# Performance work log

Measured on AMD Instinct MI355X. Metric: run time of the kernel, lower is better.

## Reference

```python
import jax, jax.numpy as jnp
import numpy as np

D = 256                      # covariance dim, hardcoded by bottleneck Conv2d(_, 256, 1)
ITER_N = 5                   # SqrtmLayer(output, 5)
_r, _c = np.triu_indices(D)
FLAT_IDX = jnp.asarray(_r * D + _c)   # upper-tri (incl. diag) indices into flattened d*d


def setup_inputs() -> dict:
    key = jax.random.key(0)
    ks = jax.random.split(key, 5)
    B, C, H, W = 64, 2048, 16, 16
    num_classes = 4
    feats = D * (D + 1) // 2  # 32896
    return {
        "features": jax.random.normal(ks[0], (B, C, H, W), jnp.float32),
        "w_bn": jax.random.normal(ks[1], (D, C), jnp.float32) * 0.02,
        "b_bn": jnp.zeros((D,), jnp.float32),
        "w_type": jax.random.normal(ks[2], (num_classes, feats), jnp.float32) * 0.01,
        "b_type": jnp.zeros((num_classes,), jnp.float32),
        "w_flag": jax.random.normal(ks[3], (1, feats), jnp.float32) * 0.01,
        "b_flag": jnp.zeros((1,), jnp.float32),
    }


def _covpool(x):
    # x: [B, d, h, w] -> second-order pooling: x_f @ I_hat @ x_f^T, equivalent
    # to (1/M) * centered @ centered^T  (I_hat = -1/M^2 * ones + 1/M * eye)
    B, d, h, w = x.shape
    M = h * w
    xf = x.reshape(B, d, M)
    centered = xf - xf.mean(axis=2, keepdims=True)
    return jnp.einsum('bim,bjm->bij', centered, centered) / M  # [B, d, d]


def _sqrtm_ns(A, iter_n=ITER_N):
    # Newton-Schulz iteration for matrix square root (iSQRT-COV style)
    B, d, _ = A.shape
    I3 = 3.0 * jnp.eye(d, dtype=A.dtype)
    normA = jnp.trace(A, axis1=1, axis2=2)          # [B], pre-normalization
    An = A / normA[:, None, None]
    ZY = 0.5 * (I3 - An)
    Y = jnp.matmul(An, ZY)
    Z = ZY
    for _ in range(iter_n - 2):
        ZY = 0.5 * (I3 - jnp.matmul(Z, Y))
        Y = jnp.matmul(Y, ZY)
        Z = jnp.matmul(ZY, Z)
    YZY = 0.5 * jnp.matmul(Y, I3 - jnp.matmul(Z, Y))
    return YZY * jnp.sqrt(normA)[:, None, None]     # post-compensation


def reference(features, w_bn, b_bn, w_type, b_type, w_flag, b_flag):
    # 1x1 bottleneck conv: [B, C, H, W] -> [B, 256, H, W]
    x = jnp.einsum('bchw,oc->bohw', features, w_bn) + b_bn[None, :, None, None]
    cov = _covpool(x)                # [B, 256, 256]
    s = _sqrtm_ns(cov)               # [B, 256, 256]
    B = s.shape[0]
    vec = s.reshape(B, D * D)[:, FLAT_IDX]   # triu-vec: [B, 32896]
    type_logits = vec @ w_type.T + b_type    # [B, num_classes]
    flag_logits = vec @ w_flag.T + b_flag    # [B, 1]
    return (type_logits, flag_logits)
```

## Files before the change

### kernel.cpp

```cpp
#include <hip/hip_runtime.h>
#include <math.h>


typedef __attribute__((ext_vector_type(8))) short bf16x8;
typedef __attribute__((ext_vector_type(4))) float f32x4;
typedef __attribute__((ext_vector_type(4))) unsigned u32x4;
typedef __attribute__((ext_vector_type(2))) unsigned u32x2;

__device__ __forceinline__ unsigned fbits(float f) { union { float f; unsigned u; } x; x.f = f; return x.u; }
__device__ __forceinline__ float bitsf(unsigned u) { union { float f; unsigned u; } x; x.u = u; return x.f; }

__device__ __forceinline__ unsigned pack_h(float a, float b) {
  return (fbits(a) >> 16) | (fbits(b) & 0xFFFF0000u);
}
__device__ __forceinline__ unsigned pack_l(float a, float b) {
  float la = a - bitsf(fbits(a) & 0xFFFF0000u);
  float lb = b - bitsf(fbits(b) & 0xFFFF0000u);
  return (fbits(la) >> 16) | (fbits(lb) & 0xFFFF0000u);
}

__device__ __forceinline__ const bf16x8* fragp(const char* M, int kt, int row,
                                               int g, int pl) {
  return (const bf16x8*)(M + (size_t)kt * 32768 + (size_t)row * 128 +
                         ((((pl << 2) + g) ^ (row & 7)) << 4));
}
__device__ __forceinline__ const bf16x8* fragl(const char* L, int kt, int row,
                                               int g, int pl) {
  return (const bf16x8*)(L + kt * 8192 + row * 128 +
                         ((((pl << 2) + g) ^ (row & 7)) << 4));
}

__device__ __forceinline__ void write_quad_g(char* M, int row, int k0,
                                             const float* v) {
  char* rp = M + (size_t)(k0 >> 5) * 32768 + (size_t)row * 128;
  const int s = (k0 & 31) >> 3, bo = (k0 & 7) * 2;
  *(u32x2*)(rp + (((s) ^ (row & 7)) << 4) + bo) =
      (u32x2){pack_h(v[0], v[1]), pack_h(v[2], v[3])};
  *(u32x2*)(rp + (((s + 4) ^ (row & 7)) << 4) + bo) =
      (u32x2){pack_l(v[0], v[1]), pack_l(v[2], v[3])};
}
__device__ __forceinline__ void write_quad_l(char* L, int row, int k0,
                                             const float* v) {
  char* rp = L + (k0 >> 5) * 8192 + row * 128;
  const int s = (k0 & 31) >> 3, bo = (k0 & 7) * 2;
  *(u32x2*)(rp + (((s) ^ (row & 7)) << 4) + bo) =
      (u32x2){pack_h(v[0], v[1]), pack_h(v[2], v[3])};
  *(u32x2*)(rp + (((s + 4) ^ (row & 7)) << 4) + bo) =
      (u32x2){pack_l(v[0], v[1]), pack_l(v[2], v[3])};
}
__device__ __forceinline__ void read_quad_g(const char* M, int row, int k0,
                                            float* v) {
  const char* rp = M + (size_t)(k0 >> 5) * 32768 + (size_t)row * 128;
  const int s = (k0 & 31) >> 3, bo = (k0 & 7) * 2;
  const u32x2 hq = *(const u32x2*)(rp + (((s) ^ (row & 7)) << 4) + bo);
  const u32x2 lq = *(const u32x2*)(rp + (((s + 4) ^ (row & 7)) << 4) + bo);
  v[0] = bitsf(hq[0] << 16) + bitsf(lq[0] << 16);
  v[1] = bitsf(hq[0] & 0xFFFF0000u) + bitsf(lq[0] & 0xFFFF0000u);
  v[2] = bitsf(hq[1] << 16) + bitsf(lq[1] << 16);
  v[3] = bitsf(hq[1] & 0xFFFF0000u) + bitsf(lq[1] & 0xFFFF0000u);
}

#define MFMA3(c, aH, aL, bH, bL)                                            \
  c = __builtin_amdgcn_mfma_f32_16x16x32_bf16(aL, bH, c, 0, 0, 0);          \
  c = __builtin_amdgcn_mfma_f32_16x16x32_bf16(aH, bL, c, 0, 0, 0);          \
  c = __builtin_amdgcn_mfma_f32_16x16x32_bf16(aH, bH, c, 0, 0, 0);

#define LGKM_BAR() do { asm volatile("s_waitcnt lgkmcnt(0)" ::: "memory"); \
                        __builtin_amdgcn_s_barrier(); } while (0)

__global__ __launch_bounds__(256) void prep_k(
    const float* __restrict__ w_bn, const float* __restrict__ w_type,
    const float* __restrict__ w_flag, char* __restrict__ Wf,
    float* __restrict__ W2)
{
  const int bid = blockIdx.x;
  if (bid < 64) {
    const int kt = bid, r = threadIdx.x;
    const float* src = w_bn + (size_t)r * 2048 + kt * 32;
    char* rp = Wf + (size_t)kt * 32768 + (size_t)r * 128;
#pragma unroll
    for (int s = 0; s < 4; ++s) {
      float x[8];
#pragma unroll
      for (int e = 0; e < 8; ++e) x[e] = src[s * 8 + e];
      *(u32x4*)(rp + ((s ^ (r & 7)) << 4)) =
          (u32x4){pack_h(x[0], x[1]), pack_h(x[2], x[3]),
                  pack_h(x[4], x[5]), pack_h(x[6], x[7])};
      *(u32x4*)(rp + (((s + 4) ^ (r & 7)) << 4)) =
          (u32x4){pack_l(x[0], x[1]), pack_l(x[2], x[3]),
                  pack_l(x[4], x[5]), pack_l(x[6], x[7])};
    }
  } else {
    const int idx = bid - 64;
    const int v = idx >> 4, chunk = idx & 15;
    const float* src = (v < 4) ? (w_type + (size_t)v * 32896) : w_flag;
    const int s0 = chunk * 4096 + threadIdx.x * 16;
    float outv[16];
#pragma unroll
    for (int q = 0; q < 16; ++q) {
      const int s = s0 + q;
      const int jbp = s >> 14, r = s & 16383;
      const int ttid = r >> 5, qq = r & 31;
      const int m = qq >> 4, n = (qq >> 2) & 3, jj = qq & 3;
      const int ww = ttid >> 6, ll = ttid & 63;
      const int i = ww * 32 + m * 16 + (ll >> 4) * 4 + jj;
      const int jcol = jbp * 64 + n * 16 + (ll & 15);
      const int rr = i < jcol ? i : jcol, cc = i < jcol ? jcol : i;
      const int t = rr * 256 - (rr * (rr - 1)) / 2 + (cc - rr);
      outv[q] = src[t] * (i == jcol ? 1.0f : 0.5f);
    }
    float* dst = W2 + (size_t)v * 65536 + s0;
#pragma unroll
    for (int q = 0; q < 4; ++q)
      *(f32x4*)(dst + q * 4) = *(f32x4*)(outv + q * 4);
  }
}

__global__ __launch_bounds__(512) void conv6_k(
    const char* __restrict__ Wf, const float* __restrict__ F,
    float* __restrict__ Xpart)
{
  __shared__ float bf32s[2][64 * 33];
  __shared__ __align__(16) char bfmt[2][2][8192];

  const int tid = threadIdx.x, lane = tid & 63, w = tid >> 6;
  const int wr = w >> 1, wc = w & 1, fr = lane & 15, g = lane >> 4;
  const int jb = blockIdx.x * 64, bz = blockIdx.y, ks = blockIdx.z;
  const int kb = ks * 32;
  const float* Fb = F + (size_t)bz * 524288;

  const int blc = tid >> 4, blpx = (tid & 15) * 4;
  const int pkpx = tid >> 3, pkq = tid & 3, pkpl = (tid >> 2) & 1;

  f32x4 acc[4][2] = {};
  bf16x8 paA[4][2], paB[4][2];

  auto bload = [&](int t) -> float4 {
    return *(const float4*)(Fb + ((size_t)(kb + t) * 32 + blc) * 256 + jb + blpx);
  };
  auto bf32w = [&](int kk, const float4& r) {
    float* p = &bf32s[kk][0];
    p[(blpx + 0) * 33 + blc] = r.x;
    p[(blpx + 1) * 33 + blc] = r.y;
    p[(blpx + 2) * 33 + blc] = r.z;
    p[(blpx + 3) * 33 + blc] = r.w;
  };
  auto aload = [&](int t, bf16x8 (*pa)[2]) {
#pragma unroll
    for (int m = 0; m < 4; ++m) {
      const int r = wr * 64 + m * 16 + fr;
#pragma unroll
      for (int pl = 0; pl < 2; ++pl) pa[m][pl] = *fragp(Wf, kb + t, r, g, pl);
    }
  };
  auto pack = [&](int kk, int dq) {
    const float* p = &bf32s[kk][pkpx * 33 + pkq * 8];
    float x[8];
#pragma unroll
    for (int e = 0; e < 8; ++e) x[e] = p[e];
    u32x4 outv;
    if (pkpl == 0)
      outv = (u32x4){pack_h(x[0], x[1]), pack_h(x[2], x[3]),
                     pack_h(x[4], x[5]), pack_h(x[6], x[7])};
    else
      outv = (u32x4){pack_l(x[0], x[1]), pack_l(x[2], x[3]),
                     pack_l(x[4], x[5]), pack_l(x[6], x[7])};
    const int slot = ((pkpl << 2) + pkq) ^ (pkpx & 7);
    *(u32x4*)(&bfmt[dq][kk][pkpx * 128 + slot * 16]) = outv;
  };
  auto gemmstep = [&](int sq, int kk, bf16x8 (*pa)[2]) {
    bf16x8 bH[2], bL[2];
#pragma unroll
    for (int n = 0; n < 2; ++n) {
      const int r = wc * 32 + n * 16 + fr;
      const char* rp = &bfmt[sq][kk][r * 128];
      bH[n] = *(const bf16x8*)(rp + ((g ^ (r & 7)) << 4));
      bL[n] = *(const bf16x8*)(rp + (((g + 4) ^ (r & 7)) << 4));
    }
#pragma unroll
    for (int m = 0; m < 4; ++m)
#pragma unroll
      for (int n = 0; n < 2; ++n) {
        f32x4 c = acc[m][n];
        MFMA3(c, pa[m][0], pa[m][1], bH[n], bL[n]);
        acc[m][n] = c;
      }
  };

  float4 b0 = bload(0), b1 = bload(1), b2 = bload(2), b3 = bload(3);
  float4 blE0 = bload(4), blE1 = bload(5);
  float4 blO0 = bload(6), blO1 = bload(7);
  aload(0, paA);
  aload(1, paB);

  bf32w(0, b0); bf32w(1, b1);
  LGKM_BAR();
  pack(0, 0); pack(1, 0);
  LGKM_BAR();
  bf32w(0, b2); bf32w(1, b3);
  LGKM_BAR();

  for (int pp = 0; pp < 8; ++pp) {
    const int k4 = 4 * pp;
    gemmstep(0, 0, paA);
    gemmstep(0, 1, paB);
    aload(k4 + 2, paA);
    aload(k4 + 3, paB);
    pack(0, 1); pack(1, 1);
    LGKM_BAR();
    if (pp < 7) { bf32w(0, blE0); bf32w(1, blE1); }
    if (pp < 6) { blE0 = bload(k4 + 8); blE1 = bload(k4 + 9); }
    LGKM_BAR();
    gemmstep(1, 0, paA);
    gemmstep(1, 1, paB);
    if (pp < 7) { aload(k4 + 4, paA); aload(k4 + 5, paB); }
    if (pp < 7) { pack(0, 0); pack(1, 0); }
    LGKM_BAR();
    if (pp < 7) { bf32w(0, blO0); bf32w(1, blO1); }
    if (pp < 6) { blO0 = bload(k4 + 10); blO1 = bload(k4 + 11); }
    LGKM_BAR();
  }

  float* Xp = Xpart + ((size_t)ks * 64 + bz) * 65536;
#pragma unroll
  for (int m = 0; m < 4; ++m) {
    const int gi0 = wr * 64 + m * 16 + g * 4;
#pragma unroll
    for (int n = 0; n < 2; ++n) {
      const int gj = jb + wc * 32 + n * 16 + fr;
#pragma unroll
      for (int j = 0; j < 4; ++j)
        Xp[(size_t)(gi0 + j) * 256 + gj] = acc[m][n][j];
    }
  }
}

__global__ __launch_bounds__(256) void combine_k(
    const float* __restrict__ Xp0, const float* __restrict__ Xp1,
    const float* __restrict__ bias, char* __restrict__ X,
    float* __restrict__ mu, float* __restrict__ nrm_part)
{
  const int chunk = blockIdx.x, bz = blockIdx.y;
  const int tid = threadIdx.x, lane = tid & 63, w = tid >> 6;
  const float* p0 = Xp0 + (size_t)bz * 65536;
  const float* p1 = Xp1 + (size_t)bz * 65536;
  char* Xb = X + (size_t)bz * 262144;
  float tracc = 0.f;
#pragma unroll
  for (int i = 0; i < 8; ++i) {
    const int r = chunk * 32 + w * 8 + i;
    const float4 a = *(const float4*)(p0 + (size_t)r * 256 + lane * 4);
    const float4 b = *(const float4*)(p1 + (size_t)r * 256 + lane * 4);
    const float bi = bias[r];
    float v[4] = {a.x + b.x + bi, a.y + b.y + bi,
                  a.z + b.z + bi, a.w + b.w + bi};
    float s = v[0] + v[1] + v[2] + v[3];
    float ss = v[0] * v[0] + v[1] * v[1] + v[2] * v[2] + v[3] * v[3];
#pragma unroll
    for (int o = 32; o > 0; o >>= 1) {
      s += __shfl_down(s, o);
      ss += __shfl_down(ss, o);
    }
    const float st = __shfl(s, 0), sst = __shfl(ss, 0);
    const float m = st * (1.f / 256.f);
    if (lane == 0) mu[bz * 256 + r] = m;
    tracc += sst * (1.f / 256.f) - m * m;
    write_quad_g(Xb, r, lane * 4, v);
  }
  __shared__ float red[4];
  if (lane == 0) red[w] = tracc;
  __syncthreads();
  if (tid == 0)
    nrm_part[bz * 8 + chunk] = red[0] + red[1] + red[2] + red[3];
}

__device__ __forceinline__ float nrm_sum(const float* nrmp, int bz) {
  float nv = 0.f;
#pragma unroll
  for (int q = 0; q < 8; ++q) nv += nrmp[bz * 8 + q];
  return nv;
}

template <int MODE>
__global__ __launch_bounds__(512) void col_k(
    const char* __restrict__ A1, const char* __restrict__ Bsrc,
    const char* __restrict__ Ys, const char* __restrict__ Zs,
    char* __restrict__ outA, char* __restrict__ outB,
    const float* __restrict__ mu, const float* __restrict__ nrmp,
    float* __restrict__ Sf)
{
  __shared__ __align__(16) char Plds[65536];
  const int tid = threadIdx.x, lane = tid & 63, w = tid >> 6;
  const int fr = lane & 15, g = lane >> 4;
  const int blk = blockIdx.x;
  const int bz = (blk & 7) * 8 + ((blk >> 3) & 7);
  const int jbp = blk >> 6;
  const int jb = jbp * 64;
  const size_t MB = 262144;
  const char* Ab = A1 + (size_t)bz * MB;
  const char* Bb = Bsrc + (size_t)bz * MB;
  const int r0 = g * 4;

  f32x4 acc[2][4] = {};
  {
    bf16x8 pa[2][2][2], pb[2][4][2];
#pragma unroll
    for (int par = 0; par < 2; ++par) {
#pragma unroll
      for (int m = 0; m < 2; ++m) {
        const int r = w * 32 + m * 16 + fr;
#pragma unroll
        for (int pl = 0; pl < 2; ++pl) pa[par][m][pl] = *fragp(Ab, par, r, g, pl);
      }
#pragma unroll
      for (int n = 0; n < 4; ++n) {
        const int r = jb + n * 16 + fr;
#pragma unroll
        for (int pl = 0; pl < 2; ++pl) pb[par][n][pl] = *fragp(Bb, par, r, g, pl);
      }
    }
    for (int t2 = 0; t2 < 8; t2 += 2) {
#pragma unroll
      for (int par = 0; par < 2; ++par) {
        const int t = t2 + par;
        bf16x8 aH[2], aL[2], bH[4], bL[4];
#pragma unroll
        for (int m = 0; m < 2; ++m) { aH[m] = pa[par][m][0]; aL[m] = pa[par][m][1]; }
#pragma unroll
        for (int n = 0; n < 4; ++n) { bH[n] = pb[par][n][0]; bL[n] = pb[par][n][1]; }
        if (t + 2 < 8) {
#pragma unroll
          for (int m = 0; m < 2; ++m) {
            const int r = w * 32 + m * 16 + fr;
#pragma unroll
            for (int pl = 0; pl < 2; ++pl)
              pa[par][m][pl] = *fragp(Ab, t + 2, r, g, pl);
          }
#pragma unroll
          for (int n = 0; n < 4; ++n) {
            const int r = jb + n * 16 + fr;
#pragma unroll
            for (int pl = 0; pl < 2; ++pl)
              pb[par][n][pl] = *fragp(Bb, t + 2, r, g, pl);
          }
        }
#pragma unroll
        for (int m = 0; m < 2; ++m)
#pragma unroll
          for (int n = 0; n < 4; ++n) {
            f32x4 c = acc[m][n];
            MFMA3(c, aH[m], aL[m], bH[n], bL[n]);
            acc[m][n] = c;
          }
      }
    }
  }

  if constexpr (MODE == 0) {
    const float rn = 1.0f / nrm_sum(nrmp, bz);
    const float* mub = mu + bz * 256;
    char* oB = outB + (size_t)bz * MB;
#pragma unroll
    for (int m = 0; m < 2; ++m) {
      const int gi0 = w * 32 + m * 16 + r0;
#pragma unroll
      for (int n = 0; n < 4; ++n) {
        const int gj = jb + n * 16 + fr;
        float zz[4];
#pragma unroll
        for (int j = 0; j < 4; ++j) {
          const float v =
              (acc[m][n][j] * (1.f / 256.f) - mub[gi0 + j] * mub[gj]) * rn;
          zz[j] = (gi0 + j == gj ? 1.5f : 0.f) - 0.5f * v;
        }
        write_quad_g(oB, gj, gi0, zz);
      }
    }
  } else if constexpr (MODE == 1) {
    char* oA = outA + (size_t)bz * MB;
#pragma unroll
    for (int m = 0; m < 2; ++m) {
      const int gi0 = w * 32 + m * 16 + r0;
#pragma unroll
      for (int n = 0; n < 4; ++n) {
        const int gj = jb + n * 16 + fr;
        float zv[4], vv[4];
        read_quad_g(Bb, gj, gi0, zv);
#pragma unroll
        for (int j = 0; j < 4; ++j) vv[j] = 3.f * zv[j] - 2.f * acc[m][n][j];
        write_quad_g(oA, gj, gi0, vv);
      }
    }
  } else {
#pragma unroll
    for (int m = 0; m < 2; ++m) {
      const int gi0 = w * 32 + m * 16 + r0;
#pragma unroll
      for (int n = 0; n < 4; ++n) {
        const int jl = n * 16 + fr;
        float vv[4] = {acc[m][n][0], acc[m][n][1], acc[m][n][2], acc[m][n][3]};
        write_quad_l(Plds, jl, gi0, vv);
      }
    }
    const char* Yb = Ys + (size_t)bz * MB;
    const char* Zb = (MODE == 2) ? (Zs + (size_t)bz * MB) : nullptr;
    bf16x8 py[2][2][2], pz[2][2][2];
#pragma unroll
    for (int par = 0; par < 2; ++par)
#pragma unroll
      for (int m = 0; m < 2; ++m) {
        const int r = w * 32 + m * 16 + fr;
#pragma unroll
        for (int pl = 0; pl < 2; ++pl) {
          py[par][m][pl] = *fragp(Yb, par, r, g, pl);
          if constexpr (MODE == 2) pz[par][m][pl] = *fragp(Zb, par, r, g, pl);
        }
      }
    __syncthreads();

    f32x4 aY[2][4] = {}, aZ[2][4] = {};
    for (int t2 = 0; t2 < 8; t2 += 2) {
#pragma unroll
      for (int par = 0; par < 2; ++par) {
        const int t = t2 + par;
        bf16x8 yH[2], yL[2], zH[2], zL[2];
#pragma unroll
        for (int m = 0; m < 2; ++m) {
          yH[m] = py[par][m][0]; yL[m] = py[par][m][1];
          if constexpr (MODE == 2) { zH[m] = pz[par][m][0]; zL[m] = pz[par][m][1]; }
        }
        if (t + 2 < 8) {
#pragma unroll
          for (int m = 0; m < 2; ++m) {
            const int r = w * 32 + m * 16 + fr;
#pragma unroll
            for (int pl = 0; pl < 2; ++pl) {
              py[par][m][pl] = *fragp(Yb, t + 2, r, g, pl);
              if constexpr (MODE == 2) pz[par][m][pl] = *fragp(Zb, t + 2, r, g, pl);
            }
          }
        }
        bf16x8 bH[4], bL[4];
#pragma unroll
        for (int n = 0; n < 4; ++n) {
          const int jl = n * 16 + fr;
          bH[n] = *fragl(Plds, t, jl, g, 0);
          bL[n] = *fragl(Plds, t, jl, g, 1);
        }
#pragma unroll
        for (int m = 0; m < 2; ++m)
#pragma unroll
          for (int n = 0; n < 4; ++n) {
            f32x4 cy = aY[m][n];
            MFMA3(cy, yH[m], yL[m], bH[n], bL[n]);
            aY[m][n] = cy;
            if constexpr (MODE == 2) {
              f32x4 cz = aZ[m][n];
              MFMA3(cz, zH[m], zL[m], bH[n], bL[n]);
              aZ[m][n] = cz;
            }
          }
      }
    }
    if constexpr (MODE == 2) {
      char* oA = outA + (size_t)bz * MB;
      char* oB = outB + (size_t)bz * MB;
#pragma unroll
      for (int m = 0; m < 2; ++m) {
        const int gi0 = w * 32 + m * 16 + r0;
#pragma unroll
        for (int n = 0; n < 4; ++n) {
          const int gj = jb + n * 16 + fr;
          float base[4], vv[4];
          read_quad_g(Yb, gj, gi0, base);
#pragma unroll
          for (int j = 0; j < 4; ++j) vv[j] = 1.5f * base[j] - 0.5f * aY[m][n][j];
          write_quad_g(oA, gj, gi0, vv);
          read_quad_g(Zb, gj, gi0, base);
#pragma unroll
          for (int j = 0; j < 4; ++j) vv[j] = 1.5f * base[j] - 0.5f * aZ[m][n][j];
          write_quad_g(oB, gj, gi0, vv);
        }
      }
    } else {
      const float sq = sqrtf(nrm_sum(nrmp, bz));
      float* Sb = Sf + (size_t)bz * 65536 + (size_t)jbp * 16384 + (size_t)tid * 32;
#pragma unroll
      for (int m = 0; m < 2; ++m) {
        const int gi0 = w * 32 + m * 16 + r0;
#pragma unroll
        for (int n = 0; n < 4; ++n) {
          const int gj = jb + n * 16 + fr;
          float base[4];
          read_quad_g(Yb, gj, gi0, base);
          f32x4 vv;
#pragma unroll
          for (int j = 0; j < 4; ++j)
            vv[j] = (1.5f * base[j] - 0.5f * aY[m][n][j]) * sq;
          *(f32x4*)(Sb + m * 16 + n * 4) = vv;
        }
      }
    }
  }
}

__global__ __launch_bounds__(256) void head2(
    const float* __restrict__ Sf, const float* __restrict__ W2,
    const float* __restrict__ b_type, const float* __restrict__ b_flag,
    float* __restrict__ out)
{
  const int b = blockIdx.x, v = blockIdx.y, tid = threadIdx.x;
  const float4* s4 = (const float4*)(Sf + (size_t)b * 65536);
  const float4* w4 = (const float4*)(W2 + (size_t)v * 65536);
  float acc = 0.f;
  for (int i = tid; i < 16384; i += 256) {
    const float4 a = s4[i], c = w4[i];
    acc += a.x * c.x + a.y * c.y + a.z * c.z + a.w * c.w;
  }
  __shared__ float red[256];
  red[tid] = acc;
  __syncthreads();
  for (int o = 128; o > 0; o >>= 1) {
    if (tid < o) red[tid] += red[tid + o];
    __syncthreads();
  }
  if (tid == 0) {
    if (v < 4) out[b * 4 + v] = red[0] + b_type[v];
    else       out[256 + b] = red[0] + b_flag[0];
  }
}

extern "C" void kernel_launch(void* const* d_in, const int* in_sizes, int n_in,
                              void* d_out, int out_size, void* d_ws, size_t ws_size,
                              hipStream_t stream)
{
  const float* features = (const float*)d_in[0];
  const float* w_bn     = (const float*)d_in[1];
  const float* b_bn     = (const float*)d_in[2];
  const float* w_type   = (const float*)d_in[3];
  const float* b_type   = (const float*)d_in[4];
  const float* w_flag   = (const float*)d_in[5];
  const float* b_flag   = (const float*)d_in[6];
  float* out = (float*)d_out;

  char* W = (char*)d_ws;
  const size_t PB = 16777216;
  char* P0 = W;           char* P1 = W + PB;     char* P2 = W + 2 * PB;
  char* P3 = W + 3 * PB;  char* P4 = W + 4 * PB;
  char* Wf = W + 5 * PB;
  float* W2 = (float*)(W + 5 * PB + 2097152);
  float* mu = (float*)(W + 5 * PB + 4194304);
  float* nrm_part = mu + 16384;
  float* Xpart = (float*)(W + 5 * PB + 8388608);
  float* Sf = (float*)P4;

  prep_k<<<dim3(144), dim3(256), 0, stream>>>(w_bn, w_type, w_flag, Wf, W2);
  conv6_k<<<dim3(4, 64, 2), dim3(512), 0, stream>>>(Wf, features, Xpart);
  combine_k<<<dim3(8, 64), dim3(256), 0, stream>>>(
      Xpart, Xpart + 64ull * 65536, b_bn, P0, mu, nrm_part);

  const dim3 cg(256), cb(512);
  col_k<0><<<cg, cb, 0, stream>>>(P0, P0, nullptr, nullptr, nullptr, P2, mu, nrm_part, nullptr);
  col_k<1><<<cg, cb, 0, stream>>>(P2, P2, nullptr, nullptr, P3, nullptr, nullptr, nullptr, nullptr);
  col_k<2><<<cg, cb, 0, stream>>>(P2, P3, P3, P2, P0, P1, nullptr, nullptr, nullptr);
  col_k<2><<<cg, cb, 0, stream>>>(P1, P0, P0, P1, P3, P2, nullptr, nullptr, nullptr);
  col_k<2><<<cg, cb, 0, stream>>>(P2, P3, P3, P2, P1, P0, nullptr, nullptr, nullptr);
  col_k<3><<<cg, cb, 0, stream>>>(P0, P1, P1, nullptr, nullptr, nullptr, nullptr, nrm_part, Sf);

  head2<<<dim3(64, 5), dim3(256), 0, stream>>>(Sf, W2, b_type, b_flag, out);
  (void)in_sizes; (void)n_in; (void)out_size; (void)ws_size;
}
```

Baseline: 268.7 us.

## Fuse Newton-Schulz chain into one cooperative kernel and raise conv split-K to four

The six separate Newton-Schulz matmul launches become one cooperative kernel that runs each stage in turn, with a grid-wide sync between stages. This removes per-launch overhead and launch gaps, but needs all 256 blocks to be resident at once. The 1x1 conv now splits K four ways instead of two, giving more blocks for parallelism. The combine kernel then has to read and sum four partial buffers, which doubles the partial-sum traffic and workspace size.

```diff
diff --git a/kernel.cpp b/kernel.cpp
--- a/kernel.cpp
+++ b/kernel.cpp
@@ -1,6 +1,9 @@
 #include <hip/hip_runtime.h>
+#include <hip/hip_cooperative_groups.h>
 #include <math.h>
 
+
+namespace cg = cooperative_groups;
 
 typedef __attribute__((ext_vector_type(8))) short bf16x8;
 typedef __attribute__((ext_vector_type(4))) float f32x4;
@@ -116,7 +119,7 @@
   }
 }
 
-__global__ __launch_bounds__(512) void conv6_k(
+__global__ __launch_bounds__(512) void conv6b_k(
     const char* __restrict__ Wf, const float* __restrict__ F,
     float* __restrict__ Xpart)
 {
@@ -126,7 +129,7 @@
   const int tid = threadIdx.x, lane = tid & 63, w = tid >> 6;
   const int wr = w >> 1, wc = w & 1, fr = lane & 15, g = lane >> 4;
   const int jb = blockIdx.x * 64, bz = blockIdx.y, ks = blockIdx.z;
-  const int kb = ks * 32;
+  const int kb = ks * 16;
   const float* Fb = F + (size_t)bz * 524288;
 
   const int blc = tid >> 4, blpx = (tid & 15) * 4;
@@ -200,7 +203,7 @@
   bf32w(0, b2); bf32w(1, b3);
   LGKM_BAR();
 
-  for (int pp = 0; pp < 8; ++pp) {
+  for (int pp = 0; pp < 4; ++pp) {
     const int k4 = 4 * pp;
     gemmstep(0, 0, paA);
     gemmstep(0, 1, paB);
@@ -208,16 +211,16 @@
     aload(k4 + 3, paB);
     pack(0, 1); pack(1, 1);
     LGKM_BAR();
-    if (pp < 7) { bf32w(0, blE0); bf32w(1, blE1); }
-    if (pp < 6) { blE0 = bload(k4 + 8); blE1 = bload(k4 + 9); }
+    if (pp < 3) { bf32w(0, blE0); bf32w(1, blE1); }
+    if (pp < 2) { blE0 = bload(k4 + 8); blE1 = bload(k4 + 9); }
     LGKM_BAR();
     gemmstep(1, 0, paA);
     gemmstep(1, 1, paB);
-    if (pp < 7) { aload(k4 + 4, paA); aload(k4 + 5, paB); }
-    if (pp < 7) { pack(0, 0); pack(1, 0); }
+    if (pp < 3) { aload(k4 + 4, paA); aload(k4 + 5, paB); }
+    if (pp < 3) { pack(0, 0); pack(1, 0); }
     LGKM_BAR();
-    if (pp < 7) { bf32w(0, blO0); bf32w(1, blO1); }
-    if (pp < 6) { blO0 = bload(k4 + 10); blO1 = bload(k4 + 11); }
+    if (pp < 3) { bf32w(0, blO0); bf32w(1, blO1); }
+    if (pp < 2) { blO0 = bload(k4 + 10); blO1 = bload(k4 + 11); }
     LGKM_BAR();
   }
 
@@ -236,24 +239,25 @@
 }
 
 __global__ __launch_bounds__(256) void combine_k(
-    const float* __restrict__ Xp0, const float* __restrict__ Xp1,
-    const float* __restrict__ bias, char* __restrict__ X,
-    float* __restrict__ mu, float* __restrict__ nrm_part)
+    const float* __restrict__ Xp, const float* __restrict__ bias,
+    char* __restrict__ X, float* __restrict__ mu, float* __restrict__ nrm_part)
 {
   const int chunk = blockIdx.x, bz = blockIdx.y;
   const int tid = threadIdx.x, lane = tid & 63, w = tid >> 6;
-  const float* p0 = Xp0 + (size_t)bz * 65536;
-  const float* p1 = Xp1 + (size_t)bz * 65536;
+  const float* p0 = Xp + (size_t)bz * 65536;
   char* Xb = X + (size_t)bz * 262144;
   float tracc = 0.f;
 #pragma unroll
   for (int i = 0; i < 8; ++i) {
     const int r = chunk * 32 + w * 8 + i;
-    const float4 a = *(const float4*)(p0 + (size_t)r * 256 + lane * 4);
-    const float4 b = *(const float4*)(p1 + (size_t)r * 256 + lane * 4);
+    const size_t off = (size_t)r * 256 + lane * 4;
+    const float4 a = *(const float4*)(p0 + off);
+    const float4 b = *(const float4*)(p0 + 64ull * 65536 + off);
+    const float4 c = *(const float4*)(p0 + 128ull * 65536 + off);
+    const float4 d = *(const float4*)(p0 + 192ull * 65536 + off);
     const float bi = bias[r];
-    float v[4] = {a.x + b.x + bi, a.y + b.y + bi,
-                  a.z + b.z + bi, a.w + b.w + bi};
+    float v[4] = {a.x + b.x + c.x + d.x + bi, a.y + b.y + c.y + d.y + bi,
+                  a.z + b.z + c.z + d.z + bi, a.w + b.w + c.w + d.w + bi};
     float s = v[0] + v[1] + v[2] + v[3];
     float ss = v[0] * v[0] + v[1] * v[1] + v[2] * v[2] + v[3] * v[3];
 #pragma unroll
@@ -281,18 +285,72 @@
   return nv;
 }
 
+__device__ __forceinline__ void stage1_gemm(
+    const char* Ab, const char* Bb, int jb, int w, int fr, int g,
+    f32x4 (&acc)[2][4])
+{
+  bf16x8 pa[2][2][2], pb[2][4][2];
+#pragma unroll
+  for (int par = 0; par < 2; ++par) {
+#pragma unroll
+    for (int m = 0; m < 2; ++m) {
+      const int r = w * 32 + m * 16 + fr;
+#pragma unroll
+      for (int pl = 0; pl < 2; ++pl) pa[par][m][pl] = *fragp(Ab, par, r, g, pl);
+    }
+#pragma unroll
+    for (int n = 0; n < 4; ++n) {
+      const int r = jb + n * 16 + fr;
+#pragma unroll
+      for (int pl = 0; pl < 2; ++pl) pb[par][n][pl] = *fragp(Bb, par, r, g, pl);
+    }
+  }
+  for (int t2 = 0; t2 < 8; t2 += 2) {
+#pragma unroll
+    for (int par = 0; par < 2; ++par) {
+      const int t = t2 + par;
+      bf16x8 aH[2], aL[2], bH[4], bL[4];
+#pragma unroll
+      for (int m = 0; m < 2; ++m) { aH[m] = pa[par][m][0]; aL[m] = pa[par][m][1]; }
+#pragma unroll
+      for (int n = 0; n < 4; ++n) { bH[n] = pb[par][n][0]; bL[n] = pb[par][n][1]; }
+      if (t + 2 < 8) {
+#pragma unroll
+        for (int m = 0; m < 2; ++m) {
+          const int r = w * 32 + m * 16 + fr;
+#pragma unroll
+          for (int pl = 0; pl < 2; ++pl)
+            pa[par][m][pl] = *fragp(Ab, t + 2, r, g, pl);
+        }
+#pragma unroll
+        for (int n = 0; n < 4; ++n) {
+          const int r = jb + n * 16 + fr;
+#pragma unroll
+          for (int pl = 0; pl < 2; ++pl)
+            pb[par][n][pl] = *fragp(Bb, t + 2, r, g, pl);
+        }
+      }
+#pragma unroll
+      for (int m = 0; m < 2; ++m)
+#pragma unroll
+        for (int n = 0; n < 4; ++n) {
+          f32x4 c = acc[m][n];
+          MFMA3(c, aH[m], aL[m], bH[n], bL[n]);
+          acc[m][n] = c;
+        }
+    }
+  }
+}
+
 template <int MODE>
-__global__ __launch_bounds__(512) void col_k(
-    const char* __restrict__ A1, const char* __restrict__ Bsrc,
-    const char* __restrict__ Ys, const char* __restrict__ Zs,
-    char* __restrict__ outA, char* __restrict__ outB,
-    const float* __restrict__ mu, const float* __restrict__ nrmp,
-    float* __restrict__ Sf)
-{
-  __shared__ __align__(16) char Plds[65536];
-  const int tid = threadIdx.x, lane = tid & 63, w = tid >> 6;
+__device__ void col_stage(
+    const char* A1, const char* Bsrc, const char* Ys, const char* Zs,
+    char* outA, char* outB, const float* mu, const float* nrmp,
+    char* Plds, int blk, int tid)
+{
+  static_assert(MODE >= 0 && MODE <= 2, "FIN handled by col_stage_fin");
+  const int lane = tid & 63, w = tid >> 6;
   const int fr = lane & 15, g = lane >> 4;
-  const int blk = blockIdx.x;
   const int bz = (blk & 7) * 8 + ((blk >> 3) & 7);
   const int jbp = blk >> 6;
   const int jb = jbp * 64;
@@ -302,59 +360,7 @@
   const int r0 = g * 4;
 
   f32x4 acc[2][4] = {};
-  {
-    bf16x8 pa[2][2][2], pb[2][4][2];
-#pragma unroll
-    for (int par = 0; par < 2; ++par) {
-#pragma unroll
-      for (int m = 0; m < 2; ++m) {
-        const int r = w * 32 + m * 16 + fr;
-#pragma unroll
-        for (int pl = 0; pl < 2; ++pl) pa[par][m][pl] = *fragp(Ab, par, r, g, pl);
-      }
-#pragma unroll
-      for (int n = 0; n < 4; ++n) {
-        const int r = jb + n * 16 + fr;
-#pragma unroll
-        for (int pl = 0; pl < 2; ++pl) pb[par][n][pl] = *fragp(Bb, par, r, g, pl);
-      }
-    }
-    for (int t2 = 0; t2 < 8; t2 += 2) {
-#pragma unroll
-      for (int par = 0; par < 2; ++par) {
-        const int t = t2 + par;
-        bf16x8 aH[2], aL[2], bH[4], bL[4];
-#pragma unroll
-        for (int m = 0; m < 2; ++m) { aH[m] = pa[par][m][0]; aL[m] = pa[par][m][1]; }
-#pragma unroll
-        for (int n = 0; n < 4; ++n) { bH[n] = pb[par][n][0]; bL[n] = pb[par][n][1]; }
-        if (t + 2 < 8) {
-#pragma unroll
-          for (int m = 0; m < 2; ++m) {
-            const int r = w * 32 + m * 16 + fr;
-#pragma unroll
-            for (int pl = 0; pl < 2; ++pl)
-              pa[par][m][pl] = *fragp(Ab, t + 2, r, g, pl);
-          }
-#pragma unroll
-          for (int n = 0; n < 4; ++n) {
-            const int r = jb + n * 16 + fr;
-#pragma unroll
-            for (int pl = 0; pl < 2; ++pl)
-              pb[par][n][pl] = *fragp(Bb, t + 2, r, g, pl);
-          }
-        }
-#pragma unroll
-        for (int m = 0; m < 2; ++m)
-#pragma unroll
-          for (int n = 0; n < 4; ++n) {
-            f32x4 c = acc[m][n];
-            MFMA3(c, aH[m], aL[m], bH[n], bL[n]);
-            acc[m][n] = c;
-          }
-      }
-    }
-  }
+  stage1_gemm(Ab, Bb, jb, w, fr, g, acc);
 
   if constexpr (MODE == 0) {
     const float rn = 1.0f / nrm_sum(nrmp, bz);
@@ -403,7 +409,7 @@
       }
     }
     const char* Yb = Ys + (size_t)bz * MB;
-    const char* Zb = (MODE == 2) ? (Zs + (size_t)bz * MB) : nullptr;
+    const char* Zb = Zs + (size_t)bz * MB;
     bf16x8 py[2][2][2], pz[2][2][2];
 #pragma unroll
     for (int par = 0; par < 2; ++par)
@@ -413,7 +419,7 @@
 #pragma unroll
         for (int pl = 0; pl < 2; ++pl) {
           py[par][m][pl] = *fragp(Yb, par, r, g, pl);
-          if constexpr (MODE == 2) pz[par][m][pl] = *fragp(Zb, par, r, g, pl);
+          pz[par][m][pl] = *fragp(Zb, par, r, g, pl);
         }
       }
     __syncthreads();
@@ -427,7 +433,7 @@
 #pragma unroll
         for (int m = 0; m < 2; ++m) {
           yH[m] = py[par][m][0]; yL[m] = py[par][m][1];
-          if constexpr (MODE == 2) { zH[m] = pz[par][m][0]; zL[m] = pz[par][m][1]; }
+          zH[m] = pz[par][m][0]; zL[m] = pz[par][m][1];
         }
         if (t + 2 < 8) {
 #pragma unroll
@@ -436,7 +442,7 @@
 #pragma unroll
             for (int pl = 0; pl < 2; ++pl) {
               py[par][m][pl] = *fragp(Yb, t + 2, r, g, pl);
-              if constexpr (MODE == 2) pz[par][m][pl] = *fragp(Zb, t + 2, r, g, pl);
+              pz[par][m][pl] = *fragp(Zb, t + 2, r, g, pl);
             }
           }
         }
@@ -454,54 +460,144 @@
             f32x4 cy = aY[m][n];
             MFMA3(cy, yH[m], yL[m], bH[n], bL[n]);
             aY[m][n] = cy;
-            if constexpr (MODE == 2) {
-              f32x4 cz = aZ[m][n];
-              MFMA3(cz, zH[m], zL[m], bH[n], bL[n]);
-              aZ[m][n] = cz;
-            }
+            f32x4 cz = aZ[m][n];
+            MFMA3(cz, zH[m], zL[m], bH[n], bL[n]);
+            aZ[m][n] = cz;
           }
       }
     }
-    if constexpr (MODE == 2) {
-      char* oA = outA + (size_t)bz * MB;
-      char* oB = outB + (size_t)bz * MB;
-#pragma unroll
-      for (int m = 0; m < 2; ++m) {
-        const int gi0 = w * 32 + m * 16 + r0;
+    char* oA = outA + (size_t)bz * MB;
+    char* oB = outB + (size_t)bz * MB;
+#pragma unroll
+    for (int m = 0; m < 2; ++m) {
+      const int gi0 = w * 32 + m * 16 + r0;
+#pragma unroll
+      for (int n = 0; n < 4; ++n) {
+        const int gj = jb + n * 16 + fr;
+        float base[4], vv[4];
+        read_quad_g(Yb, gj, gi0, base);
+#pragma unroll
+        for (int j = 0; j < 4; ++j) vv[j] = 1.5f * base[j] - 0.5f * aY[m][n][j];
+        write_quad_g(oA, gj, gi0, vv);
+        read_quad_g(Zb, gj, gi0, base);
+#pragma unroll
+        for (int j = 0; j < 4; ++j) vv[j] = 1.5f * base[j] - 0.5f * aZ[m][n][j];
+        write_quad_g(oB, gj, gi0, vv);
+      }
+    }
+  }
+}
+
+__device__ void col_stage_fin(
+    const char* A1, const char* Ys, const float* nrmp, float* Sf,
+    char* Plds, int blk, int tid)
+{
+  const int lane = tid & 63, w = tid >> 6;
+  const int fr = lane & 15, g = lane >> 4;
+  const int bz = (blk & 7) * 8 + ((blk >> 3) & 7);
+  const int jbp = blk >> 6;
+  const int jb = jbp * 64;
+  const size_t MB = 262144;
+  const char* Ab = A1 + (size_t)bz * MB;
+  const char* Bb = Ys + (size_t)bz * MB;
+  const int r0 = g * 4;
+
+  f32x4 acc[2][4] = {};
+  stage1_gemm(Ab, Bb, jb, w, fr, g, acc);
+
+#pragma unroll
+  for (int m = 0; m < 2; ++m) {
+    const int gi0 = w * 32 + m * 16 + r0;
+#pragma unroll
+    for (int n = 0; n < 4; ++n) {
+      const int jl = n * 16 + fr;
+      float vv[4] = {acc[m][n][0], acc[m][n][1], acc[m][n][2], acc[m][n][3]};
+      write_quad_l(Plds, jl, gi0, vv);
+    }
+  }
+  const char* Yb = Bb;
+  bf16x8 py[2][2][2];
+#pragma unroll
+  for (int par = 0; par < 2; ++par)
+#pragma unroll
+    for (int m = 0; m < 2; ++m) {
+      const int r = w * 32 + m * 16 + fr;
+#pragma unroll
+      for (int pl = 0; pl < 2; ++pl) py[par][m][pl] = *fragp(Yb, par, r, g, pl);
+    }
+  __syncthreads();
+
+  f32x4 aY[2][4] = {};
+  for (int t2 = 0; t2 < 8; t2 += 2) {
+#pragma unroll
+    for (int par = 0; par < 2; ++par) {
+      const int t = t2 + par;
+      bf16x8 yH[2], yL[2];
+#pragma unroll
+      for (int m = 0; m < 2; ++m) { yH[m] = py[par][m][0]; yL[m] = py[par][m][1]; }
+      if (t + 2 < 8) {
+#pragma unroll
+        for (int m = 0; m < 2; ++m) {
+          const int r = w * 32 + m * 16 + fr;
+#pragma unroll
+          for (int pl = 0; pl < 2; ++pl) py[par][m][pl] = *fragp(Yb, t + 2, r, g, pl);
+        }
+      }
+      bf16x8 bH[4], bL[4];
+#pragma unroll
+      for (int n = 0; n < 4; ++n) {
+        const int jl = n * 16 + fr;
+        bH[n] = *fragl(Plds, t, jl, g, 0);
+        bL[n] = *fragl(Plds, t, jl, g, 1);
+      }
+#pragma unroll
+      for (int m = 0; m < 2; ++m)
 #pragma unroll
         for (int n = 0; n < 4; ++n) {
-          const int gj = jb + n * 16 + fr;
-          float base[4], vv[4];
-          read_quad_g(Yb, gj, gi0, base);
-#pragma unroll
-          for (int j = 0; j < 4; ++j) vv[j] = 1.5f * base[j] - 0.5f * aY[m][n][j];
-          write_quad_g(oA, gj, gi0, vv);
-          read_quad_g(Zb, gj, gi0, base);
-#pragma unroll
-          for (int j = 0; j < 4; ++j) vv[j] = 1.5f * base[j] - 0.5f * aZ[m][n][j];
-          write_quad_g(oB, gj, gi0, vv);
-        }
-      }
-    } else {
-      const float sq = sqrtf(nrm_sum(nrmp, bz));
-      float* Sb = Sf + (size_t)bz * 65536 + (size_t)jbp * 16384 + (size_t)tid * 32;
-#pragma unroll
-      for (int m = 0; m < 2; ++m) {
-        const int gi0 = w * 32 + m * 16 + r0;
-#pragma unroll
-        for (int n = 0; n < 4; ++n) {
-          const int gj = jb + n * 16 + fr;
-          float base[4];
-          read_quad_g(Yb, gj, gi0, base);
-          f32x4 vv;
-#pragma unroll
-          for (int j = 0; j < 4; ++j)
-            vv[j] = (1.5f * base[j] - 0.5f * aY[m][n][j]) * sq;
-          *(f32x4*)(Sb + m * 16 + n * 4) = vv;
-        }
-      }
-    }
-  }
+          f32x4 cy = aY[m][n];
+          MFMA3(cy, yH[m], yL[m], bH[n], bL[n]);
+          aY[m][n] = cy;
+        }
+    }
+  }
+  const float sq = sqrtf(nrm_sum(nrmp, bz));
+  float* Sb = Sf + (size_t)bz * 65536 + (size_t)jbp * 16384 + (size_t)tid * 32;
+#pragma unroll
+  for (int m = 0; m < 2; ++m) {
+    const int gi0 = w * 32 + m * 16 + r0;
+#pragma unroll
+    for (int n = 0; n < 4; ++n) {
+      const int gj = jb + n * 16 + fr;
+      float base[4];
+      read_quad_g(Yb, gj, gi0, base);
+      f32x4 vv;
+#pragma unroll
+      for (int j = 0; j < 4; ++j)
+        vv[j] = (1.5f * base[j] - 0.5f * aY[m][n][j]) * sq;
+      *(f32x4*)(Sb + m * 16 + n * 4) = vv;
+    }
+  }
+}
+
+__global__ __launch_bounds__(512) void ns_chain_k(
+    char* P0, char* P1, char* P2, char* P3,
+    const float* mu, const float* nrmp, float* Sf)
+{
+  __shared__ __align__(16) char Plds[65536];
+  cg::grid_group grid = cg::this_grid();
+  const int blk = blockIdx.x, tid = threadIdx.x;
+
+  col_stage<0>(P0, P0, nullptr, nullptr, nullptr, P2, mu, nrmp, Plds, blk, tid);
+  grid.sync();
+  col_stage<1>(P2, P2, nullptr, nullptr, P3, nullptr, mu, nrmp, Plds, blk, tid);
+  grid.sync();
+  col_stage<2>(P2, P3, P3, P2, P0, P1, mu, nrmp, Plds, blk, tid);
+  grid.sync();
+  col_stage<2>(P1, P0, P0, P1, P3, P2, mu, nrmp, Plds, blk, tid);
+  grid.sync();
+  col_stage<2>(P2, P3, P3, P2, P1, P0, mu, nrmp, Plds, blk, tid);
+  grid.sync();
+  col_stage_fin(P0, P1, nrmp, Sf, Plds, blk, tid);
 }
 
 __global__ __launch_bounds__(256) void head2(
@@ -555,17 +651,16 @@
   float* Sf = (float*)P4;
 
   prep_k<<<dim3(144), dim3(256), 0, stream>>>(w_bn, w_type, w_flag, Wf, W2);
-  conv6_k<<<dim3(4, 64, 2), dim3(512), 0, stream>>>(Wf, features, Xpart);
-  combine_k<<<dim3(8, 64), dim3(256), 0, stream>>>(
-      Xpart, Xpart + 64ull * 65536, b_bn, P0, mu, nrm_part);
-
-  const dim3 cg(256), cb(512);
-  col_k<0><<<cg, cb, 0, stream>>>(P0, P0, nullptr, nullptr, nullptr, P2, mu, nrm_part, nullptr);
-  col_k<1><<<cg, cb, 0, stream>>>(P2, P2, nullptr, nullptr, P3, nullptr, nullptr, nullptr, nullptr);
-  col_k<2><<<cg, cb, 0, stream>>>(P2, P3, P3, P2, P0, P1, nullptr, nullptr, nullptr);
-  col_k<2><<<cg, cb, 0, stream>>>(P1, P0, P0, P1, P3, P2, nullptr, nullptr, nullptr);
-  col_k<2><<<cg, cb, 0, stream>>>(P2, P3, P3, P2, P1, P0, nullptr, nullptr, nullptr);
-  col_k<3><<<cg, cb, 0, stream>>>(P0, P1, P1, nullptr, nullptr, nullptr, nullptr, nrm_part, Sf);
+  conv6b_k<<<dim3(4, 64, 4), dim3(512), 0, stream>>>(Wf, features, Xpart);
+  combine_k<<<dim3(8, 64), dim3(256), 0, stream>>>(Xpart, b_bn, P0, mu, nrm_part);
+
+  {
+    char* p0 = P0; char* p1 = P1; char* p2 = P2; char* p3 = P3;
+    const float* mu_ = mu; const float* nr_ = nrm_part; float* sf_ = Sf;
+    void* kargs[] = {&p0, &p1, &p2, &p3, (void*)&mu_, (void*)&nr_, &sf_};
+    (void)hipLaunchCooperativeKernel((void*)ns_chain_k, dim3(256), dim3(512),
+                                     kargs, 0, stream);
+  }
 
   head2<<<dim3(64, 5), dim3(256), 0, stream>>>(Sf, W2, b_type, b_flag, out);
   (void)in_sizes; (void)n_in; (void)out_size; (void)ws_size;
```

Result: slower. 537.6 us (+100.1%).
